# Kernel tuning notes

Measured on AMD Instinct MI355X. Metric: run time of the kernel, lower is better.

## Reference

```python
import jax, jax.numpy as jnp
import numpy as np

T = 0.12  # softmax temperature


def _mlp(x, Wa, ba, Wb, bb, Wc, bc):
    # Linear -> ReLU -> (Dropout=id in eval) -> Linear -> ReLU -> Linear -> ReLU
    h = jax.nn.relu(x @ Wa + ba)
    h = jax.nn.relu(h @ Wb + bb)
    return jax.nn.relu(h @ Wc + bc)


def setup_inputs() -> dict:
    key = jax.random.key(0)
    ks = jax.random.split(key, 16)
    B, K, A, P = 2048, 64, 312, 128
    std = 0.01  # torch init: normal(0, 0.01), bias 0
    inp = {
        "v2s": jax.random.normal(ks[0], (B, A), jnp.float32),
        "tar_atts": jax.random.uniform(ks[1], (B, 1), jnp.float32),
        "sample_indices": jax.random.randint(ks[2], (B, K), 0, B),
        # CLproject[1]: 1 -> 1024 -> 2048 -> 312
        "W2a": std * jax.random.normal(ks[3], (1, 1024), jnp.float32),
        "b2a": jnp.zeros((1024,), jnp.float32),
        "W2b": std * jax.random.normal(ks[4], (1024, 2048), jnp.float32),
        "b2b": jnp.zeros((2048,), jnp.float32),
        "W2c": std * jax.random.normal(ks[5], (2048, A), jnp.float32),
        "b2c": jnp.zeros((A,), jnp.float32),
        # CLproject[0]: 312 -> 1024 -> 2048 -> 128
        "W1a": std * jax.random.normal(ks[6], (A, 1024), jnp.float32),
        "b1a": jnp.zeros((1024,), jnp.float32),
        "W1b": std * jax.random.normal(ks[7], (1024, 2048), jnp.float32),
        "b1b": jnp.zeros((2048,), jnp.float32),
        "W1c": std * jax.random.normal(ks[8], (2048, P), jnp.float32),
        "b1c": jnp.zeros((P,), jnp.float32),
    }
    return inp


def reference(v2s, tar_atts, sample_indices, W2a, b2a, W2b, b2b, W2c, b2c,
              W1a, b1a, W1b, b1b, W1c, b1c):
    # attribute embedding via CLproject[1]: [B,1] -> [B,312]
    att = _mlp(tar_atts, W2a, b2a, W2b, b2b, W2c, b2c)
    v2s_sg = jax.lax.stop_gradient(v2s)  # detach().clone()
    # gather padded pos+neg sample lists: [B,K,312]
    samples = v2s_sg[sample_indices]
    # per-sample projection via CLproject[0]
    proj_samples = _mlp(samples + att[:, None, :], W1a, b1a, W1b, b1b, W1c, b1c)  # [B,K,128]
    query = _mlp(v2s_sg + att, W1a, b1a, W1b, b1b, W1c, b1c)  # [B,128]
    # batched version of per-sample einsum('c,kc->k')
    logits = jnp.einsum("bc,bkc->bk", query, proj_samples) / T
    return logits
```

## Files before the change

### kernel.cpp

```cpp
#include <hip/hip_runtime.h>
#include <stdio.h>
#include <stdint.h>

typedef __attribute__((ext_vector_type(8))) short short8;
typedef __attribute__((ext_vector_type(4))) float f32x4;
typedef __attribute__((ext_vector_type(4))) unsigned short ushort4v;

__device__ __forceinline__ unsigned short f2bf(float f) {
  unsigned int u = __builtin_bit_cast(unsigned int, f);
  u = u + 0x7FFFu + ((u >> 16) & 1u);
  return (unsigned short)(u >> 16);
}
__device__ __forceinline__ float bf2f(unsigned short h) {
  unsigned int u = ((unsigned int)h) << 16;
  return __builtin_bit_cast(float, u);
}

__device__ __forceinline__ void gl_lds16(const unsigned short* g, unsigned short* l) {
  __builtin_amdgcn_global_load_lds(
      (const __attribute__((address_space(1))) unsigned int*)(const void*)g,
      (__attribute__((address_space(3))) unsigned int*)(void*)l, 16, 0, 0);
}

__global__ void k_transpose_cast_t(const float* __restrict__ in, unsigned short* __restrict__ out,
                                   int Nin, int Kin, int ldo) {
  __shared__ float lds[64][65];
  int k0 = blockIdx.x * 64, n0 = blockIdx.y * 64;
  int t = threadIdx.x, tc = t & 15, tr = t >> 4;
  #pragma unroll
  for (int rr = 0; rr < 4; ++rr) {
    int kl = tr + rr * 16, k = k0 + kl;
    #pragma unroll
    for (int j = 0; j < 4; ++j) {
      int nl = tc * 4 + j, n = n0 + nl;
      lds[kl][nl] = (k < Kin && n < Nin) ? in[(size_t)k * Nin + n] : 0.f;
    }
  }
  __syncthreads();
  #pragma unroll
  for (int rr = 0; rr < 4; ++rr) {
    int nl = tr + rr * 16, n = n0 + nl;
    int kb = k0 + tc * 4;
    if (kb + 3 < ldo) {
      ushort4v o;
      o.x = f2bf(lds[tc * 4 + 0][nl]);
      o.y = f2bf(lds[tc * 4 + 1][nl]);
      o.z = f2bf(lds[tc * 4 + 2][nl]);
      o.w = f2bf(lds[tc * 4 + 3][nl]);
      *(ushort4v*)&out[(size_t)n * ldo + kb] = o;
    } else {
      for (int j = 0; j < 4; ++j)
        if (kb + j < ldo) out[(size_t)n * ldo + kb + j] = f2bf(lds[tc * 4 + j][nl]);
    }
  }
}

__global__ void k_att_l1(const float* __restrict__ tar, const float* __restrict__ W2a,
                         const float* __restrict__ b2a, unsigned short* __restrict__ out) {
  int id = blockIdx.x * 256 + threadIdx.x;
  int b = id >> 10, j = id & 1023;
  out[id] = f2bf(fmaxf(tar[b] * W2a[j] + b2a[j], 0.f));
}

__global__ void k_v2s_cast(const float* __restrict__ v2s, unsigned short* __restrict__ out) {
  int id = blockIdx.x * 256 + threadIdx.x;
  int r = id / 320, c = id - r * 320;
  out[id] = (c < 312) ? f2bf(v2s[(size_t)r * 312 + c]) : (unsigned short)0;
}

__device__ __forceinline__ int lds_off(int row, int g) {
  int slot = (g + (row >> 1)) & 3;
  return row * 32 + slot * 8;
}

template<bool RELU, bool OUTBF16>
__global__ __launch_bounds__(256)
void k_gemm_bt(const unsigned short* __restrict__ A, const unsigned short* __restrict__ B,
               const float* __restrict__ bias, int bias_n, int nNt, int N_store, int K,
               void* __restrict__ outp, int ldo, int remap) {
  __shared__ __align__(16) unsigned short As[2][4096];
  __shared__ __align__(16) unsigned short Bs[2][4096];
  int d = blockIdx.x, nwg = gridDim.x;
  int L = d;
  if (remap) { int q = nwg >> 3; L = (d & 7) * q + (d >> 3); }
  int mt = L / nNt, nt = L - mt * nNt;
  size_t m0 = (size_t)mt * 128, n0 = (size_t)nt * 128;
  int tid = threadIdx.x, lane = tid & 63;
  int w = tid >> 6, wr = w >> 1, wc = w & 1;
  int sr = tid >> 2;
  int gch = ((tid & 3) - (tid >> 3)) & 3;
  const unsigned short* pA0 = A + (m0 + sr) * K + gch * 8;
  const unsigned short* pA1 = pA0 + (size_t)64 * K;
  const unsigned short* pB0 = B + (n0 + sr) * K + gch * 8;
  const unsigned short* pB1 = pB0 + (size_t)64 * K;
  int sd = (tid & ~63) * 8;

  int kg = lane >> 4, l15 = lane & 15;
  int aoff = lds_off(wr * 64 + l15, kg);
  int boff = lds_off(wc * 64 + l15, kg);

  f32x4 acc[4][4];
  #pragma unroll
  for (int i = 0; i < 4; ++i)
    #pragma unroll
    for (int j = 0; j < 4; ++j) acc[i][j] = (f32x4)(0.f);

  const int NT = K >> 5;
#define STAGE(t_, b_) do { int k0_ = (t_) * 32;                       \
    gl_lds16(pA0 + k0_, &As[b_][sd]);                                 \
    gl_lds16(pA1 + k0_, &As[b_][2048 + sd]);                          \
    gl_lds16(pB0 + k0_, &Bs[b_][sd]);                                 \
    gl_lds16(pB1 + k0_, &Bs[b_][2048 + sd]);                          \
  } while (0)

  STAGE(0, 0);
  for (int t = 0; t < NT; ++t) {
    int b = t & 1;
    __syncthreads();
    if (t + 1 < NT) STAGE(t + 1, b ^ 1);
    short8 af[4], bfr[4];
    #pragma unroll
    for (int mi = 0; mi < 4; ++mi) af[mi] = *(const short8*)&As[b][aoff + mi * 512];
    #pragma unroll
    for (int ni = 0; ni < 4; ++ni) bfr[ni] = *(const short8*)&Bs[b][boff + ni * 512];
    #pragma unroll
    for (int mi = 0; mi < 4; ++mi)
      #pragma unroll
      for (int ni = 0; ni < 4; ++ni)
        acc[mi][ni] = __builtin_amdgcn_mfma_f32_16x16x32_bf16(af[mi], bfr[ni], acc[mi][ni], 0, 0, 0);
  }
#undef STAGE

  #pragma unroll
  for (int ni = 0; ni < 4; ++ni) {
    int colg = (int)n0 + wc * 64 + ni * 16 + l15;
    if (colg < N_store) {
      float bs = bias ? (colg < bias_n ? bias[colg] : 0.f) : 0.f;
      #pragma unroll
      for (int mi = 0; mi < 4; ++mi) {
        #pragma unroll
        for (int r2 = 0; r2 < 4; ++r2) {
          size_t rowg = m0 + wr * 64 + mi * 16 + kg * 4 + r2;
          float v = acc[mi][ni][r2] + bs;
          if (RELU) v = fmaxf(v, 0.f);
          if (OUTBF16) ((unsigned short*)outp)[rowg * ldo + colg] = f2bf(v);
          else         ((float*)outp)[rowg * ldo + colg] = v;
        }
      }
    }
  }
}

__global__ void k_build_h1(const float* __restrict__ V1, const float* __restrict__ A1p,
                           const int* __restrict__ idx, unsigned short* __restrict__ H1c,
                           int rbase) {
  int row = rbase + blockIdx.x;
  int src, arow;
  if (row < 2048) { src = row; arow = row; }
  else {
    int g = row - 2048; arow = g >> 6;
    int s = idx[g];
    src = s < 0 ? 0 : (s > 2047 ? 2047 : s);
  }
  int j = threadIdx.x * 4;
  float4 v = *(const float4*)(V1 + (size_t)src * 1024 + j);
  float4 a = *(const float4*)(A1p + (size_t)arow * 1024 + j);
  ushort4v o;
  o.x = f2bf(fmaxf(v.x + a.x, 0.f));
  o.y = f2bf(fmaxf(v.y + a.y, 0.f));
  o.z = f2bf(fmaxf(v.z + a.z, 0.f));
  o.w = f2bf(fmaxf(v.w + a.w, 0.f));
  *(ushort4v*)(H1c + (size_t)blockIdx.x * 1024 + j) = o;
}

__global__ void k_dot(const unsigned short* __restrict__ P, float* __restrict__ out) {
  __shared__ float q[128];
  int b = blockIdx.x, t = threadIdx.x;
  if (t < 128) q[t] = bf2f(P[(size_t)b * 128 + t]);
  __syncthreads();
  int k = t >> 2, part = t & 3;
  const unsigned short* row = P + (size_t)(2048 + b * 64 + k) * 128 + part * 32;
  const float* qp = q + part * 32;
  float s = 0.f;
  #pragma unroll
  for (int j = 0; j < 32; j += 8) {
    short8 pv = *(const short8*)(row + j);
    #pragma unroll
    for (int e = 0; e < 8; ++e)
      s += bf2f((unsigned short)pv[e]) * qp[j + e];
  }
  s += __shfl_xor(s, 1);
  s += __shfl_xor(s, 2);
  if (part == 0) out[(size_t)b * 64 + k] = s * (float)(1.0 / 0.12);
}

extern "C" void kernel_launch(void* const* d_in, const int* in_sizes, int n_in,
                              void* d_out, int out_size, void* d_ws, size_t ws_size,
                              hipStream_t stream) {
  const float* v2s = (const float*)d_in[0];
  const float* tar = (const float*)d_in[1];
  const int*   sidx = (const int*)d_in[2];
  const float* W2a = (const float*)d_in[3];
  const float* b2a = (const float*)d_in[4];
  const float* W2b = (const float*)d_in[5];
  const float* b2b = (const float*)d_in[6];
  const float* W2c = (const float*)d_in[7];
  const float* b2c = (const float*)d_in[8];
  const float* W1a = (const float*)d_in[9];
  const float* b1a = (const float*)d_in[10];
  const float* W1b = (const float*)d_in[11];
  const float* b1b = (const float*)d_in[12];
  const float* W1c = (const float*)d_in[13];
  const float* b1c = (const float*)d_in[14];
  float* out = (float*)d_out;

  char* ws = (char*)d_ws;
  size_t off = 0;
  auto alloc = [&](size_t bytes) -> char* {
    char* p = ws + off; off += (bytes + 255) & ~(size_t)255; return p;
  };
  unsigned short* W1bT = (unsigned short*)alloc(2048ull * 1024 * 2);
  unsigned short* W1cT = (unsigned short*)alloc(128ull * 2048 * 2);
  float*          V1   = (float*)alloc(2048ull * 1024 * 4);
  float*          A1p  = (float*)alloc(2048ull * 1024 * 4);
  unsigned short* Pb   = (unsigned short*)alloc(133120ull * 128 * 2);
  size_t O = off;
  off = O;
  unsigned short* W1aT = (unsigned short*)alloc(1024ull * 320 * 2);
  unsigned short* v2sb = (unsigned short*)alloc(2048ull * 320 * 2);
  unsigned short* attb = (unsigned short*)alloc(2048ull * 320 * 2);
  unsigned short* W2bT = (unsigned short*)alloc(2048ull * 1024 * 2);
  unsigned short* W2cT = (unsigned short*)alloc(384ull * 2048 * 2);
  unsigned short* h_a  = (unsigned short*)alloc(2048ull * 1024 * 2);
  unsigned short* h2a  = (unsigned short*)alloc(2048ull * 2048 * 2);
  size_t early_end = off;

  static const int plans[4][8] = {{260,260,0,0,0,0,0,0},
                                  {132,132,128,128,0,0,0,0},
                                  {130,130,130,130,0,0,0,0},
                                  {65,65,65,65,65,65,65,65}};
  int sel = -1, maxmt = 0;
  for (int p = 0; p < 4 && sel < 0; ++p) {
    int mx = 0;
    for (int i = 0; i < 8; ++i) if (plans[p][i] > mx) mx = plans[p][i];
    size_t rows = (size_t)mx * 256;
    size_t late = O + ((rows * 1024 * 2 + 255) & ~(size_t)255)
                    + ((rows * 2048 * 2 + 255) & ~(size_t)255);
    size_t need = late > early_end ? late : early_end;
    if (need <= ws_size) { sel = p; maxmt = mx; }
  }
  int fallR = 0;
  if (sel < 0) {
    size_t rows = 133120ull / 16;
    size_t late = O + ((rows * 1024 * 2 + 255) & ~(size_t)255)
                    + ((rows * 2048 * 2 + 255) & ~(size_t)255);
    size_t need = late > early_end ? late : early_end;
    if (need <= ws_size) fallR = (int)rows;
  }
  fprintf(stderr, "[kernel_launch] ws_size=%zu sel=%d\n", ws_size, sel);
  if (sel < 0 && !fallR) {
    hipMemsetAsync(d_out, 0, (size_t)out_size * 4, stream);
    return;
  }
  off = O;
  size_t bufrows = (sel >= 0) ? (size_t)maxmt * 256 : (size_t)fallR;
  unsigned short* H1c = (unsigned short*)alloc(bufrows * 1024 * 2);
  unsigned short* H2c = (unsigned short*)alloc(bufrows * 2048 * 2);

  dim3 blk(256);
  k_transpose_cast_t<<<dim3(16, 32), blk, 0, stream>>>(W2b, W2bT, 2048, 1024, 1024);
  k_transpose_cast_t<<<dim3(32, 6),  blk, 0, stream>>>(W2c, W2cT, 312, 2048, 2048);
  k_transpose_cast_t<<<dim3(5, 16),  blk, 0, stream>>>(W1a, W1aT, 1024, 312, 320);
  k_transpose_cast_t<<<dim3(16, 32), blk, 0, stream>>>(W1b, W1bT, 2048, 1024, 1024);
  k_transpose_cast_t<<<dim3(32, 2),  blk, 0, stream>>>(W1c, W1cT, 128, 2048, 2048);
  k_att_l1<<<8192, blk, 0, stream>>>(tar, W2a, b2a, h_a);
  k_v2s_cast<<<2560, blk, 0, stream>>>(v2s, v2sb);
  k_gemm_bt<true,  true ><<<256, blk, 0, stream>>>(h_a,  W2bT, b2b, 2048, 16, 2048, 1024, h2a,  2048, 1);
  k_gemm_bt<true,  true ><<<48,  blk, 0, stream>>>(h2a,  W2cT, b2c, 312,  3,  320,  2048, attb, 320,  1);
  k_gemm_bt<false, false><<<128, blk, 0, stream>>>(v2sb, W1aT, nullptr, 0,  8, 1024, 320, V1,  1024, 1);
  k_gemm_bt<false, false><<<128, blk, 0, stream>>>(attb, W1aT, b1a, 1024,  8, 1024, 320, A1p, 1024, 1);
  if (sel >= 0) {
    int rbase = 0;
    for (int i = 0; i < 8 && plans[sel][i]; ++i) {
      int R = plans[sel][i] * 256;
      k_build_h1<<<R, blk, 0, stream>>>(V1, A1p, sidx, H1c, rbase);
      k_gemm_bt<true, true><<<(R / 128) * 16, blk, 0, stream>>>(H1c, W1bT, b1b, 2048, 16, 2048, 1024, H2c, 2048, 1);
      k_gemm_bt<true, true><<<(R / 128), blk, 0, stream>>>(H2c, W1cT, b1c, 128, 1, 128, 2048,
                                                            Pb + (size_t)rbase * 128, 128, 0);
      rbase += R;
    }
  } else {
    for (int c = 0; c < 16; ++c) {
      int rbase = c * fallR;
      k_build_h1<<<fallR, blk, 0, stream>>>(V1, A1p, sidx, H1c, rbase);
      k_gemm_bt<true, true><<<(fallR / 128) * 16, blk, 0, stream>>>(H1c, W1bT, b1b, 2048, 16, 2048, 1024, H2c, 2048, 1);
      k_gemm_bt<true, true><<<(fallR / 128), blk, 0, stream>>>(H2c, W1cT, b1c, 128, 1, 128, 2048,
                                                                Pb + (size_t)rbase * 128, 128, 0);
    }
  }
  k_dot<<<2048, blk, 0, stream>>>(Pb, out);
}
```

Baseline: 1.076 ms.

## Triple-buffer GEMM LDS staging with register prefetch and raw barriers

Replaces the double-buffered GEMM main loop with a three-stage LDS ring, staging two tiles ahead. LDS fragments for the next tile are read into registers while the current tile's MFMAs run. __syncthreads is replaced by explicit vmcnt/lgkmcnt waits and raw s_barrier, and s_setprio is raised around the MFMA block. This aims to hide global-to-LDS latency and LDS read latency behind compute, at the cost of more LDS (48KB), extra registers, and fragile hand-managed wait counts.

```diff
diff --git a/kernel.cpp b/kernel.cpp
--- a/kernel.cpp
+++ b/kernel.cpp
@@ -21,6 +21,10 @@
       (const __attribute__((address_space(1))) unsigned int*)(const void*)g,
       (__attribute__((address_space(3))) unsigned int*)(void*)l, 16, 0, 0);
 }
+
+#define RAW_BAR()  asm volatile("s_barrier" ::: "memory")
+#define LGKM0()    asm volatile("s_waitcnt lgkmcnt(0)" ::: "memory")
+#define VMCNT(n_)  asm volatile("s_waitcnt vmcnt(" #n_ ")" ::: "memory")
 
 __global__ void k_transpose_cast_t(const float* __restrict__ in, unsigned short* __restrict__ out,
                                    int Nin, int Kin, int ldo) {
@@ -78,8 +82,8 @@
 void k_gemm_bt(const unsigned short* __restrict__ A, const unsigned short* __restrict__ B,
                const float* __restrict__ bias, int bias_n, int nNt, int N_store, int K,
                void* __restrict__ outp, int ldo, int remap) {
-  __shared__ __align__(16) unsigned short As[2][4096];
-  __shared__ __align__(16) unsigned short Bs[2][4096];
+  __shared__ __align__(16) unsigned short As[3][4096];
+  __shared__ __align__(16) unsigned short Bs[3][4096];
   int d = blockIdx.x, nwg = gridDim.x;
   int L = d;
   if (remap) { int q = nwg >> 3; L = (d & 7) * q + (d >> 3); }
@@ -112,24 +116,48 @@
     gl_lds16(pB0 + k0_, &Bs[b_][sd]);                                 \
     gl_lds16(pB1 + k0_, &Bs[b_][2048 + sd]);                          \
   } while (0)
-
-  STAGE(0, 0);
-  for (int t = 0; t < NT; ++t) {
-    int b = t & 1;
-    __syncthreads();
-    if (t + 1 < NT) STAGE(t + 1, b ^ 1);
-    short8 af[4], bfr[4];
-    #pragma unroll
-    for (int mi = 0; mi < 4; ++mi) af[mi] = *(const short8*)&As[b][aoff + mi * 512];
-    #pragma unroll
-    for (int ni = 0; ni < 4; ++ni) bfr[ni] = *(const short8*)&Bs[b][boff + ni * 512];
-    #pragma unroll
-    for (int mi = 0; mi < 4; ++mi)
-      #pragma unroll
-      for (int ni = 0; ni < 4; ++ni)
-        acc[mi][ni] = __builtin_amdgcn_mfma_f32_16x16x32_bf16(af[mi], bfr[ni], acc[mi][ni], 0, 0, 0);
+#define READF(b_, fa_, fb_) do {                                                  \
+    _Pragma("unroll")                                                             \
+    for (int mi = 0; mi < 4; ++mi) fa_[mi] = *(const short8*)&As[b_][aoff + mi * 512]; \
+    _Pragma("unroll")                                                             \
+    for (int ni = 0; ni < 4; ++ni) fb_[ni] = *(const short8*)&Bs[b_][boff + ni * 512]; \
+  } while (0)
+#define MFMAC(fa_, fb_) do {                                                      \
+    __builtin_amdgcn_s_setprio(1);                                                \
+    _Pragma("unroll")                                                             \
+    for (int mi = 0; mi < 4; ++mi)                                                \
+      _Pragma("unroll")                                                           \
+      for (int ni = 0; ni < 4; ++ni)                                              \
+        acc[mi][ni] = __builtin_amdgcn_mfma_f32_16x16x32_bf16(fa_[mi], fb_[ni], acc[mi][ni], 0, 0, 0); \
+    __builtin_amdgcn_s_setprio(0);                                                \
+  } while (0)
+
+  STAGE(0, 0); STAGE(1, 1); STAGE(2, 2);
+  VMCNT(4); RAW_BAR();
+  short8 ea[4], ebv[4], oa[4], obv[4];
+  READF(0, ea, ebv);
+  LGKM0();
+  RAW_BAR();
+
+  int bA = 0, bB = 1, bC = 2;
+  for (int t = 0; t < NT; t += 2) {
+    if (t + 3 < NT) STAGE(t + 3, bA);
+    if (t + 1 < NT) READF(bB, oa, obv);
+    MFMAC(ea, ebv);
+    LGKM0();
+    if (t + 3 < NT) { VMCNT(4); } else { VMCNT(0); }
+    RAW_BAR();
+    if (t + 4 < NT) STAGE(t + 4, bB);
+    if (t + 2 < NT) READF(bC, ea, ebv);
+    MFMAC(oa, obv);
+    LGKM0();
+    if (t + 4 < NT) { VMCNT(4); } else { VMCNT(0); }
+    RAW_BAR();
+    int tmp = bC; bC = bB; bB = bA; bA = tmp;
   }
 #undef STAGE
+#undef READF
+#undef MFMAC
 
   #pragma unroll
   for (int ni = 0; ni < 4; ++ni) {
```

Result: slower. 1.259 ms (+17.0%).

## Add specialized 128x128 GEMM with 64-wide K tiles for the dominant layer

Applied to the files above, without the earlier changes.

Adds a dedicated bf16 MFMA GEMM kernel for the big 1024->2048 sample-projection layer. It stages 64-wide K tiles through double-buffered, XOR-swizzled LDS using direct global-to-LDS loads, and remaps workgroup IDs across 8 groups for better cache locality. The bias and ReLU epilogue is hardcoded with no bounds checks. The aim is fewer barriers per K and better LDS bandwidth on the hottest GEMM, at the cost of more LDS per block (64 KB) and possibly lower occupancy.

```diff
diff --git a/kernel.cpp b/kernel.cpp
--- a/kernel.cpp
+++ b/kernel.cpp
@@ -16,10 +16,10 @@
   return __builtin_bit_cast(float, u);
 }
 
-__device__ __forceinline__ void gl_lds16(const unsigned short* g, unsigned short* l) {
+__device__ __forceinline__ void gl_lds16(const void* g, void* l) {
   __builtin_amdgcn_global_load_lds(
-      (const __attribute__((address_space(1))) unsigned int*)(const void*)g,
-      (__attribute__((address_space(3))) unsigned int*)(void*)l, 16, 0, 0);
+      (const __attribute__((address_space(1))) unsigned int*)g,
+      (__attribute__((address_space(3))) unsigned int*)l, 16, 0, 0);
 }
 
 __global__ void k_transpose_cast_t(const float* __restrict__ in, unsigned short* __restrict__ out,
@@ -151,6 +151,98 @@
   }
 }
 
+__global__ __launch_bounds__(256)
+void k_gemm64(const unsigned short* __restrict__ A, const unsigned short* __restrict__ B,
+              const float* __restrict__ bias, int nNt, int K,
+              unsigned short* __restrict__ outp, int ldo) {
+  __shared__ __align__(16) unsigned short As[2][8192];
+  __shared__ __align__(16) unsigned short Bs[2][8192];
+  int d = blockIdx.x, nwg = gridDim.x;
+  int q = nwg >> 3;
+  int L = (d & 7) * q + (d >> 3);
+  int mt = L / nNt, nt = L - mt * nNt;
+  size_t m0 = (size_t)mt * 128, n0 = (size_t)nt * 128;
+  int tid = threadIdx.x, lane = tid & 63;
+  int w = tid >> 6, wr = w >> 1, wc = w & 1;
+
+  int l3 = lane >> 3, s8 = lane & 7;
+  const unsigned short* pA[4];
+  const unsigned short* pB[4];
+  int sdst[4];
+  #pragma unroll
+  for (int j = 0; j < 4; ++j) {
+    int row = w * 32 + j * 8 + l3;
+    int g = (s8 - (row >> 1)) & 7;
+    pA[j] = A + (m0 + row) * K + g * 8;
+    pB[j] = B + (n0 + row) * K + g * 8;
+    sdst[j] = (w * 4 + j) * 512;
+  }
+
+  int kg = lane >> 4, l15 = lane & 15;
+  int ra = wr * 64 + l15, rb = wc * 64 + l15;
+  int aoffs[2], boffs[2];
+  #pragma unroll
+  for (int ks = 0; ks < 2; ++ks) {
+    aoffs[ks] = ra * 64 + ((ks * 4 + kg + (ra >> 1)) & 7) * 8;
+    boffs[ks] = rb * 64 + ((ks * 4 + kg + (rb >> 1)) & 7) * 8;
+  }
+
+  f32x4 acc[4][4];
+  #pragma unroll
+  for (int i = 0; i < 4; ++i)
+    #pragma unroll
+    for (int j = 0; j < 4; ++j) acc[i][j] = (f32x4)(0.f);
+
+  const int NT = K >> 6;
+#define STAGE64(t_, b_) do { int k0_ = (t_) * 64;                     \
+    _Pragma("unroll")                                                 \
+    for (int j = 0; j < 4; ++j) {                                     \
+      gl_lds16(pA[j] + k0_, &As[b_][sdst[j]]);                        \
+      gl_lds16(pB[j] + k0_, &Bs[b_][sdst[j]]);                        \
+    }                                                                 \
+  } while (0)
+
+  STAGE64(0, 0);
+  for (int t = 0; t < NT; ++t) {
+    int b = t & 1;
+    __syncthreads();
+    if (t + 1 < NT) STAGE64(t + 1, b ^ 1);
+    short8 af[4][2], bfr[4][2];
+    #pragma unroll
+    for (int mi = 0; mi < 4; ++mi)
+      #pragma unroll
+      for (int ks = 0; ks < 2; ++ks)
+        af[mi][ks] = *(const short8*)&As[b][aoffs[ks] + mi * 1024];
+    #pragma unroll
+    for (int ni = 0; ni < 4; ++ni)
+      #pragma unroll
+      for (int ks = 0; ks < 2; ++ks)
+        bfr[ni][ks] = *(const short8*)&Bs[b][boffs[ks] + ni * 1024];
+    #pragma unroll
+    for (int mi = 0; mi < 4; ++mi)
+      #pragma unroll
+      for (int ni = 0; ni < 4; ++ni)
+        #pragma unroll
+        for (int ks = 0; ks < 2; ++ks)
+          acc[mi][ni] = __builtin_amdgcn_mfma_f32_16x16x32_bf16(af[mi][ks], bfr[ni][ks], acc[mi][ni], 0, 0, 0);
+  }
+#undef STAGE64
+
+  #pragma unroll
+  for (int ni = 0; ni < 4; ++ni) {
+    int colg = (int)n0 + wc * 64 + ni * 16 + l15;
+    float bs = bias[colg];
+    #pragma unroll
+    for (int mi = 0; mi < 4; ++mi) {
+      #pragma unroll
+      for (int r2 = 0; r2 < 4; ++r2) {
+        size_t rowg = m0 + wr * 64 + mi * 16 + kg * 4 + r2;
+        outp[rowg * ldo + colg] = f2bf(fmaxf(acc[mi][ni][r2] + bs, 0.f));
+      }
+    }
+  }
+}
+
 __global__ void k_build_h1(const float* __restrict__ V1, const float* __restrict__ A1p,
                            const int* __restrict__ idx, unsigned short* __restrict__ H1c,
                            int rbase) {
@@ -284,7 +376,7 @@
     for (int i = 0; i < 8 && plans[sel][i]; ++i) {
       int R = plans[sel][i] * 256;
       k_build_h1<<<R, blk, 0, stream>>>(V1, A1p, sidx, H1c, rbase);
-      k_gemm_bt<true, true><<<(R / 128) * 16, blk, 0, stream>>>(H1c, W1bT, b1b, 2048, 16, 2048, 1024, H2c, 2048, 1);
+      k_gemm64<<<(R / 128) * 16, blk, 0, stream>>>(H1c, W1bT, b1b, 16, 1024, H2c, 2048);
       k_gemm_bt<true, true><<<(R / 128), blk, 0, stream>>>(H2c, W1cT, b1c, 128, 1, 128, 2048,
                                                             Pb + (size_t)rbase * 128, 128, 0);
       rbase += R;
@@ -293,7 +385,7 @@
     for (int c = 0; c < 16; ++c) {
       int rbase = c * fallR;
       k_build_h1<<<fallR, blk, 0, stream>>>(V1, A1p, sidx, H1c, rbase);
-      k_gemm_bt<true, true><<<(fallR / 128) * 16, blk, 0, stream>>>(H1c, W1bT, b1b, 2048, 16, 2048, 1024, H2c, 2048, 1);
+      k_gemm64<<<(fallR / 128) * 16, blk, 0, stream>>>(H1c, W1bT, b1b, 16, 1024, H2c, 2048);
       k_gemm_bt<true, true><<<(fallR / 128), blk, 0, stream>>>(H2c, W1cT, b1c, 128, 1, 128, 2048,
                                                                 Pb + (size_t)rbase * 128, 128, 0);
     }
```

After: 1.066 ms. Within noise of the previous version (-0.9%).
